# Optimization experiments

Hardware: AMD Instinct MI355X
Metric: run time of the kernel (lower is better)

## Reference

```python
import jax, jax.numpy as jnp
import numpy as np

BOHR_RADIUS = 0.529177  # Angstrom
KE_KCAL = 332.0636      # Coulomb constant, kcal/mol * Angstrom / e^2
EPS = 1e-15
R_CUT = 5.0

ZBL = {'d': [0.8854 * BOHR_RADIUS], 'z_exp': [0.23],
       'c': [0.1818, 0.5099, 0.2802, 0.02817],
       'exponents': [3.2, 0.9423, 0.4028, 0.2016]}

def _inv_softplus(v):
    v = np.asarray(v, dtype=np.float32)
    return jnp.asarray(np.log(np.exp(v) - 1.0).reshape(-1, 1))

def setup_inputs() -> dict:
    key = jax.random.key(0)
    k1, k2, k3, k4 = jax.random.split(key, 4)
    N, E, M = 200000, 8000000, 1000
    xyz = jax.random.normal(k1, (N, 3), dtype=jnp.float32) * 3.0
    z = jax.random.randint(k2, (N,), 1, 94, dtype=jnp.int32)
    nbrs = jax.random.randint(k3, (E, 2), 0, N, dtype=jnp.int32)
    offsets = jax.random.normal(k4, (E, 3), dtype=jnp.float32) * 2.0
    num_atoms = jnp.full((M,), N // M, dtype=jnp.int32)
    return {
        'xyz': xyz, 'z': z, 'nbrs': nbrs, 'num_atoms': num_atoms, 'offsets': offsets,
        'd_inv': _inv_softplus(ZBL['d']),
        'z_exp_inv': _inv_softplus(ZBL['z_exp']),
        'c_inv': _inv_softplus(ZBL['c']),
        'exponents_inv': _inv_softplus(ZBL['exponents']),
    }

def reference(xyz, z, nbrs, num_atoms, offsets, d_inv, z_exp_inv, c_inv, exponents_inv):
    sp = jax.nn.softplus
    d, z_exp, c, exponents = sp(d_inv), sp(z_exp_inv), sp(c_inv), sp(exponents_inv)

    i, j = nbrs[:, 0], nbrs[:, 1]
    mask = j > i  # undirected-edge filter (masked instead of gathered: same math)

    z_i = z[i].astype(jnp.float32)  # [E]
    z_j = z[j].astype(jnp.float32)
    diff = xyz[i] - xyz[j] - offsets                  # [E,3]
    r_ij = jnp.sqrt((diff ** 2 + EPS).sum(-1))        # stable norm, [E]

    # ZBL phi: d,z_exp are [1,1]; broadcast over edges
    a = (d / (z_i ** z_exp + z_j ** z_exp)).reshape(-1)           # [E]
    phi = (c * jnp.exp(-exponents * r_ij / a)).sum(0) / c.sum()   # [4,E] -> [E]

    # SpookyNet cutoff, NaN-safe outside r_cut
    den = (R_CUT - r_ij) * (R_CUT + r_ij)
    safe_den = jnp.where(r_ij < R_CUT, den, 1.0)
    f_cut = jnp.where(r_ij < R_CUT, jnp.exp(-r_ij ** 2 / safe_den), 0.0)

    pairwise = KE_KCAL * z_i * z_j / r_ij * phi * f_cut
    pairwise = jnp.where(mask, pairwise, 0.0)

    N = xyz.shape[0]
    M = num_atoms.shape[0]
    mol_idx = jnp.repeat(jnp.arange(M), num_atoms, total_repeat_length=N)  # [N]
    seg = mol_idx[i]                                                       # [E]
    energy = jax.ops.segment_sum(pairwise, seg, num_segments=M).reshape(-1, 1)
    return energy
```

## Files before the change

kernel.cpp:

```cpp
#include <hip/hip_runtime.h>
#include <hip/hip_bf16.h>

#define R_CUT_F  5.0f
#define KE_F     332.0636f
#define MAX_M    1024

__device__ __forceinline__ float softplusf(float x) {
    return logf(1.0f + expf(x));
}

__global__ void scan_zero_kernel(const int* __restrict__ num_atoms, int M,
                                 int* __restrict__ mol_starts,
                                 float* __restrict__ out) {
    __shared__ int buf[MAX_M];
    int t = threadIdx.x;
    buf[t] = (t < M) ? num_atoms[t] : 0;
    __syncthreads();
    for (int off = 1; off < MAX_M; off <<= 1) {
        int x = (t >= off) ? buf[t - off] : 0;
        __syncthreads();
        buf[t] += x;
        __syncthreads();
    }
    if (t == 0) mol_starts[0] = 0;
    if (t < M) mol_starts[t + 1] = buf[t];
    for (int k = t; k < M; k += blockDim.x) out[k] = 0.0f;
}

__global__ void fill_mol_kernel(const int* __restrict__ mol_starts,
                                int* __restrict__ mol_idx, int M, int N) {
    int m = blockIdx.x;
    int s = mol_starts[m];
    int e = (m == M - 1) ? N : mol_starts[m + 1];
    if (e > N) e = N;
    for (int a = s + (int)threadIdx.x; a < e; a += (int)blockDim.x)
        mol_idx[a] = m;
}

__global__ __launch_bounds__(256) void nr_main_kernel(
    const float* __restrict__ xyz, const int* __restrict__ z,
    const int* __restrict__ nbrs, const float* __restrict__ offsets,
    const int* __restrict__ mol_idx,
    const float* __restrict__ d_inv, const float* __restrict__ z_exp_inv,
    const float* __restrict__ c_inv, const float* __restrict__ exp_inv,
    float* __restrict__ out, int E, int M) {
    __shared__ float sm[MAX_M];
    for (int t = threadIdx.x; t < MAX_M; t += blockDim.x) sm[t] = 0.0f;
    __syncthreads();

    const float dd    = softplusf(d_inv[0]);
    const float zexp  = softplusf(z_exp_inv[0]);
    const float c0 = softplusf(c_inv[0]);
    const float c1 = softplusf(c_inv[1]);
    const float c2 = softplusf(c_inv[2]);
    const float c3 = softplusf(c_inv[3]);
    const float e0 = softplusf(exp_inv[0]);
    const float e1 = softplusf(exp_inv[1]);
    const float e2 = softplusf(exp_inv[2]);
    const float e3 = softplusf(exp_inv[3]);
    const float inv_csum = 1.0f / (c0 + c1 + c2 + c3);
    const float inv_d    = 1.0f / dd;

    const int stride = gridDim.x * blockDim.x;
    for (int e = blockIdx.x * blockDim.x + threadIdx.x; e < E; e += stride) {
        const int2 ij = ((const int2*)nbrs)[e];
        const int i = ij.x, j = ij.y;
        if (j <= i) continue;

        const float ox = offsets[3 * e + 0];
        const float oy = offsets[3 * e + 1];
        const float oz = offsets[3 * e + 2];
        const float dx = xyz[3 * i + 0] - xyz[3 * j + 0] - ox;
        const float dy = xyz[3 * i + 1] - xyz[3 * j + 1] - oy;
        const float dz = xyz[3 * i + 2] - xyz[3 * j + 2] - oz;
        const float r2 = dx * dx + dy * dy + dz * dz + 3e-15f;
        const float r  = sqrtf(r2);
        if (r >= R_CUT_F) continue;

        const float zi = (float)z[i];
        const float zj = (float)z[j];
        const float S  = __powf(zi, zexp) + __powf(zj, zexp);
        const float t  = r * S * inv_d;
        const float phi = (c0 * __expf(-e0 * t) + c1 * __expf(-e1 * t) +
                           c2 * __expf(-e2 * t) + c3 * __expf(-e3 * t)) * inv_csum;
        const float fcut = __expf(-r2 / (25.0f - r2));
        const float val  = KE_F * zi * zj * phi * fcut / r;

        atomicAdd(&sm[mol_idx[i]], val);
    }
    __syncthreads();
    for (int t = threadIdx.x; t < M; t += blockDim.x) {
        const float v = sm[t];
        if (v != 0.0f) atomicAdd(&out[t], v);
    }
}

extern "C" void kernel_launch(void* const* d_in, const int* in_sizes, int n_in,
                              void* d_out, int out_size, void* d_ws, size_t ws_size,
                              hipStream_t stream) {
    const float* xyz       = (const float*)d_in[0];
    const int*   z         = (const int*)d_in[1];
    const int*   nbrs      = (const int*)d_in[2];
    const int*   num_atoms = (const int*)d_in[3];
    const float* offsets   = (const float*)d_in[4];
    const float* d_inv     = (const float*)d_in[5];
    const float* z_exp_inv = (const float*)d_in[6];
    const float* c_inv     = (const float*)d_in[7];
    const float* exp_inv   = (const float*)d_in[8];
    float* out = (float*)d_out;

    const int N = in_sizes[0] / 3;
    const int E = in_sizes[2] / 2;
    const int M = in_sizes[3];

    int* mol_starts = (int*)d_ws;
    int* mol_idx    = mol_starts + ((M + 1 + 3) & ~3);

    scan_zero_kernel<<<1, MAX_M, 0, stream>>>(num_atoms, M, mol_starts, out);
    fill_mol_kernel<<<M, 64, 0, stream>>>(mol_starts, mol_idx, M, N);
    nr_main_kernel<<<1024, 256, 0, stream>>>(xyz, z, nbrs, offsets, mol_idx,
                                             d_inv, z_exp_inv, c_inv, exp_inv,
                                             out, E, M);
}
```

Before: 290.6 us.

## Pack per-atom data into float4/float2 and replace global atomics with partial reduction

Precomputes per-atom packed records (xyz plus z as float4, and z^zexp plus molecule index as float2) so each edge needs fewer, wider gathers. Edge-invariant parameters are precomputed once in a setup kernel, the cutoff test now runs on r2 before the sqrt, and the edge stream is read with nontemporal loads. Global atomics are replaced by per-block partial arrays that a separate reduce kernel sums deterministically, and the grid grows to 2048 blocks. This adds a pack pass over N atoms and a partial buffer of nblk×1024 floats that must be written and re-read. If the workspace is too small, nblk falls back to fewer blocks.

```diff
diff --git a/kernel.cpp b/kernel.cpp
--- a/kernel.cpp
+++ b/kernel.cpp
@@ -1,17 +1,22 @@
 #include <hip/hip_runtime.h>
 #include <hip/hip_bf16.h>
 
-#define R_CUT_F  5.0f
 #define KE_F     332.0636f
 #define MAX_M    1024
+#define BLK      256
+#define NBLK_MAX 2048
 
 __device__ __forceinline__ float softplusf(float x) {
     return logf(1.0f + expf(x));
 }
 
-__global__ void scan_zero_kernel(const int* __restrict__ num_atoms, int M,
-                                 int* __restrict__ mol_starts,
-                                 float* __restrict__ out) {
+__global__ void scan_params_kernel(const int* __restrict__ num_atoms, int M,
+                                   const float* __restrict__ d_inv,
+                                   const float* __restrict__ z_exp_inv,
+                                   const float* __restrict__ c_inv,
+                                   const float* __restrict__ exp_inv,
+                                   int* __restrict__ mol_starts,
+                                   float* __restrict__ params) {
     __shared__ int buf[MAX_M];
     int t = threadIdx.x;
     buf[t] = (t < M) ? num_atoms[t] : 0;
@@ -24,74 +29,115 @@
     }
     if (t == 0) mol_starts[0] = 0;
     if (t < M) mol_starts[t + 1] = buf[t];
-    for (int k = t; k < M; k += blockDim.x) out[k] = 0.0f;
+    if (t == 0) {
+        float dd = softplusf(d_inv[0]);
+        float c0 = softplusf(c_inv[0]), c1 = softplusf(c_inv[1]);
+        float c2 = softplusf(c_inv[2]), c3 = softplusf(c_inv[3]);
+        float e0 = softplusf(exp_inv[0]), e1 = softplusf(exp_inv[1]);
+        float e2 = softplusf(exp_inv[2]), e3 = softplusf(exp_inv[3]);
+        float ic = 1.0f / (c0 + c1 + c2 + c3);
+        float id = 1.0f / dd;
+        params[0] = c0 * ic; params[1] = c1 * ic; params[2] = c2 * ic; params[3] = c3 * ic;
+        params[4] = e0 * id; params[5] = e1 * id; params[6] = e2 * id; params[7] = e3 * id;
+        params[8] = softplusf(z_exp_inv[0]);
+    }
 }
 
-__global__ void fill_mol_kernel(const int* __restrict__ mol_starts,
-                                int* __restrict__ mol_idx, int M, int N) {
-    int m = blockIdx.x;
-    int s = mol_starts[m];
-    int e = (m == M - 1) ? N : mol_starts[m + 1];
-    if (e > N) e = N;
-    for (int a = s + (int)threadIdx.x; a < e; a += (int)blockDim.x)
-        mol_idx[a] = m;
+__global__ void pack_kernel(const float* __restrict__ xyz,
+                            const int* __restrict__ z,
+                            const int* __restrict__ mol_starts, int M, int N,
+                            const float* __restrict__ params,
+                            float4* __restrict__ pack,
+                            float2* __restrict__ aux) {
+    int a = blockIdx.x * blockDim.x + threadIdx.x;
+    if (a >= N) return;
+    float zf = (float)z[a];
+    pack[a] = make_float4(xyz[3 * a + 0], xyz[3 * a + 1], xyz[3 * a + 2], zf);
+    int lo = 0, hi = M;
+    while (hi - lo > 1) {
+        int mid = (lo + hi) >> 1;
+        if (mol_starts[mid] <= a) lo = mid; else hi = mid;
+    }
+    aux[a] = make_float2(__powf(zf, params[8]), __int_as_float(lo));
 }
 
 __global__ __launch_bounds__(256) void nr_main_kernel(
-    const float* __restrict__ xyz, const int* __restrict__ z,
-    const int* __restrict__ nbrs, const float* __restrict__ offsets,
-    const int* __restrict__ mol_idx,
-    const float* __restrict__ d_inv, const float* __restrict__ z_exp_inv,
-    const float* __restrict__ c_inv, const float* __restrict__ exp_inv,
-    float* __restrict__ out, int E, int M) {
+    const long long* __restrict__ nbrs,
+    const float* __restrict__ offsets,
+    const float4* __restrict__ pack,
+    const float2* __restrict__ aux,
+    const float* __restrict__ params,
+    float* __restrict__ part, int E) {
     __shared__ float sm[MAX_M];
-    for (int t = threadIdx.x; t < MAX_M; t += blockDim.x) sm[t] = 0.0f;
+    for (int t = threadIdx.x; t < MAX_M; t += BLK) sm[t] = 0.0f;
     __syncthreads();
 
-    const float dd    = softplusf(d_inv[0]);
-    const float zexp  = softplusf(z_exp_inv[0]);
-    const float c0 = softplusf(c_inv[0]);
-    const float c1 = softplusf(c_inv[1]);
-    const float c2 = softplusf(c_inv[2]);
-    const float c3 = softplusf(c_inv[3]);
-    const float e0 = softplusf(exp_inv[0]);
-    const float e1 = softplusf(exp_inv[1]);
-    const float e2 = softplusf(exp_inv[2]);
-    const float e3 = softplusf(exp_inv[3]);
-    const float inv_csum = 1.0f / (c0 + c1 + c2 + c3);
-    const float inv_d    = 1.0f / dd;
+    const float4 kk = *(const float4*)(params + 0);
+    const float4 gg = *(const float4*)(params + 4);
 
-    const int stride = gridDim.x * blockDim.x;
-    for (int e = blockIdx.x * blockDim.x + threadIdx.x; e < E; e += stride) {
-        const int2 ij = ((const int2*)nbrs)[e];
-        const int i = ij.x, j = ij.y;
+    const int stride = gridDim.x * BLK;
+    for (int e = blockIdx.x * BLK + threadIdx.x; e < E; e += stride) {
+        const long long nb = __builtin_nontemporal_load(nbrs + e);
+        const int i = (int)nb;
+        const int j = (int)(nb >> 32);
         if (j <= i) continue;
 
-        const float ox = offsets[3 * e + 0];
-        const float oy = offsets[3 * e + 1];
-        const float oz = offsets[3 * e + 2];
-        const float dx = xyz[3 * i + 0] - xyz[3 * j + 0] - ox;
-        const float dy = xyz[3 * i + 1] - xyz[3 * j + 1] - oy;
-        const float dz = xyz[3 * i + 2] - xyz[3 * j + 2] - oz;
-        const float r2 = dx * dx + dy * dy + dz * dz + 3e-15f;
-        const float r  = sqrtf(r2);
-        if (r >= R_CUT_F) continue;
+        const float ox = __builtin_nontemporal_load(offsets + 3 * e + 0);
+        const float oy = __builtin_nontemporal_load(offsets + 3 * e + 1);
+        const float oz = __builtin_nontemporal_load(offsets + 3 * e + 2);
+        const float4 pi = pack[i];
+        const float4 pj = pack[j];
+        const float dx = pi.x - pj.x - ox;
+        const float dy = pi.y - pj.y - oy;
+        const float dz = pi.z - pj.z - oz;
+        const float r2 = fmaf(dx, dx, fmaf(dy, dy, dz * dz)) + 3e-15f;
+        if (r2 >= 25.0f) continue;
 
-        const float zi = (float)z[i];
-        const float zj = (float)z[j];
-        const float S  = __powf(zi, zexp) + __powf(zj, zexp);
-        const float t  = r * S * inv_d;
-        const float phi = (c0 * __expf(-e0 * t) + c1 * __expf(-e1 * t) +
-                           c2 * __expf(-e2 * t) + c3 * __expf(-e3 * t)) * inv_csum;
-        const float fcut = __expf(-r2 / (25.0f - r2));
-        const float val  = KE_F * zi * zj * phi * fcut / r;
+        const float inv_r = rsqrtf(r2);
+        const float r = r2 * inv_r;
+        const float2 ai = aux[i];
+        const float2 aj = aux[j];
+        const float rs = r * (ai.x + aj.x);
+        const float phi = kk.x * __expf(-gg.x * rs) + kk.y * __expf(-gg.y * rs) +
+                          kk.z * __expf(-gg.z * rs) + kk.w * __expf(-gg.w * rs);
+        const float fcut = __expf(-__fdividef(r2, 25.0f - r2));
+        const float val = KE_F * pi.w * pj.w * inv_r * phi * fcut;
 
-        atomicAdd(&sm[mol_idx[i]], val);
+        atomicAdd(&sm[__float_as_int(ai.y)], val);
     }
     __syncthreads();
-    for (int t = threadIdx.x; t < M; t += blockDim.x) {
-        const float v = sm[t];
-        if (v != 0.0f) atomicAdd(&out[t], v);
+    const float4* sm4 = (const float4*)sm;
+    float4* dst = (float4*)(part + (size_t)blockIdx.x * MAX_M);
+    dst[threadIdx.x] = sm4[threadIdx.x];
+}
+
+__global__ void reduce_kernel(const float* __restrict__ part, int nblk,
+                              float* __restrict__ out, int M) {
+    __shared__ float4 smr[BLK];
+    const int q = blockIdx.x;
+    float4 acc = make_float4(0.f, 0.f, 0.f, 0.f);
+    for (int b = threadIdx.x; b < nblk; b += BLK) {
+        const float4 v = *(const float4*)(part + (size_t)b * MAX_M + 4 * q);
+        acc.x += v.x; acc.y += v.y; acc.z += v.z; acc.w += v.w;
+    }
+    smr[threadIdx.x] = acc;
+    __syncthreads();
+    for (int s = BLK / 2; s > 0; s >>= 1) {
+        if (threadIdx.x < s) {
+            smr[threadIdx.x].x += smr[threadIdx.x + s].x;
+            smr[threadIdx.x].y += smr[threadIdx.x + s].y;
+            smr[threadIdx.x].z += smr[threadIdx.x + s].z;
+            smr[threadIdx.x].w += smr[threadIdx.x + s].w;
+        }
+        __syncthreads();
+    }
+    if (threadIdx.x == 0) {
+        const int m = 4 * q;
+        const float4 r = smr[0];
+        if (m + 0 < M) out[m + 0] = r.x;
+        if (m + 1 < M) out[m + 1] = r.y;
+        if (m + 2 < M) out[m + 2] = r.z;
+        if (m + 3 < M) out[m + 3] = r.w;
     }
 }
 
@@ -113,12 +159,28 @@
     const int E = in_sizes[2] / 2;
     const int M = in_sizes[3];
 
-    int* mol_starts = (int*)d_ws;
-    int* mol_idx    = mol_starts + ((M + 1 + 3) & ~3);
+    char* w = (char*)d_ws;
+    int*    mol_starts = (int*)w;
+    float*  params     = (float*)(w + 4096);
+    float4* pack       = (float4*)(w + 8192);
+    float2* aux        = (float2*)(w + 8192 + 16 * (size_t)N);
+    size_t  part_off   = 8192 + 24 * (size_t)N;
+    float*  part       = (float*)(w + part_off);
 
-    scan_zero_kernel<<<1, MAX_M, 0, stream>>>(num_atoms, M, mol_starts, out);
-    fill_mol_kernel<<<M, 64, 0, stream>>>(mol_starts, mol_idx, M, N);
-    nr_main_kernel<<<1024, 256, 0, stream>>>(xyz, z, nbrs, offsets, mol_idx,
-                                             d_inv, z_exp_inv, c_inv, exp_inv,
-                                             out, E, M);
+    int nblk = NBLK_MAX;
+    if (ws_size > part_off) {
+        size_t maxb = (ws_size - part_off) / (sizeof(float) * MAX_M);
+        if ((size_t)nblk > maxb) nblk = (int)maxb;
+    } else {
+        nblk = 1;
+    }
+    if (nblk < 1) nblk = 1;
+
+    scan_params_kernel<<<1, MAX_M, 0, stream>>>(num_atoms, M, d_inv, z_exp_inv,
+                                                c_inv, exp_inv, mol_starts, params);
+    pack_kernel<<<(N + BLK - 1) / BLK, BLK, 0, stream>>>(xyz, z, mol_starts, M, N,
+                                                         params, pack, aux);
+    nr_main_kernel<<<nblk, BLK, 0, stream>>>((const long long*)nbrs, offsets,
+                                             pack, aux, params, part, E);
+    reduce_kernel<<<(M + 3) / 4, BLK, 0, stream>>>(part, nblk, out, M);
 }
```

Result: faster. 277.2 us (-4.6%).
